# Kernel tuning notes

Hardware: AMD Instinct MI355X
Metric: run time of the kernel (lower is better)

The kernel has to match this reference:

```python
import jax, jax.numpy as jnp
import numpy as np

N_NODES = 20000
N_EDGES = 320000
MUL = 64            # multiplicity of 0e and 1o in hidden/out irreps
NUM_BASIS = 8
INV_SQRT3 = 0.5773502691896258
EPS = 1e-5


def setup_inputs() -> dict:
    key = jax.random.key(0)
    k = jax.random.split(key, 16)
    return {
        "node_hiddens": jax.random.normal(k[0], (N_NODES, 4 * MUL), dtype=jnp.float32),
        "edge_attr": jax.random.uniform(k[1], (N_EDGES, NUM_BASIS), dtype=jnp.float32),
        "edge_sh": jax.random.normal(k[2], (N_EDGES, 4), dtype=jnp.float32),
        "w1_s": jax.random.normal(k[3], (MUL, MUL), dtype=jnp.float32),
        "w1_v": jax.random.normal(k[4], (MUL, MUL), dtype=jnp.float32),
        "wsc_s": jax.random.normal(k[5], (MUL, MUL), dtype=jnp.float32),
        "wsc_v": jax.random.normal(k[6], (MUL, MUL), dtype=jnp.float32),
        "w2_s": jax.random.normal(k[7], (2 * MUL, MUL), dtype=jnp.float32),
        "w2_v": jax.random.normal(k[8], (2 * MUL, MUL), dtype=jnp.float32),
        "fc_w1": jax.random.normal(k[9], (NUM_BASIS, 64), dtype=jnp.float32),
        "fc_w2": jax.random.normal(k[10], (64, 64), dtype=jnp.float32),
        "fc_w3": jax.random.normal(k[11], (64, 4 * MUL), dtype=jnp.float32),
        "g_s": jnp.ones((MUL,), dtype=jnp.float32),
        "g_v": jnp.ones((MUL,), dtype=jnp.float32),
        "edge_index": jax.random.randint(k[12], (2, N_EDGES), 0, N_NODES),
    }


def reference(node_hiddens, edge_attr, edge_sh, w1_s, w1_v, wsc_s, wsc_v,
              w2_s, w2_v, fc_w1, fc_w2, fc_w3, g_s, g_v, edge_index):
    N = node_hiddens.shape[0]
    # e3nn layout: [N, 64x0e | 64x1o] with mul-major vectors
    xs = node_hiddens[:, :MUL]                        # [N, 64]
    xv = node_hiddens[:, MUL:].reshape(N, MUL, 3)     # [N, 64, 3]

    # edge MLP (FullyConnectedNet([8,64,64,256], silu)) -> per-edge TP weights
    h = jax.nn.silu(edge_attr @ fc_w1 * (1.0 / np.sqrt(float(NUM_BASIS))))
    h = jax.nn.silu(h @ fc_w2 * (1.0 / np.sqrt(64.0)))
    w = h @ fc_w3 * (1.0 / np.sqrt(64.0))             # [E, 4*MUL]
    wA, wB, wC, wD = jnp.split(w, 4, axis=1)          # one 64-vec per uvu path

    inv = 1.0 / np.sqrt(float(MUL))
    # self-connection Linear(hidden -> out)
    sc_s = xs @ wsc_s * inv
    sc_v = jnp.einsum('nud,uv->nvd', xv, wsc_v) * inv
    # linear_1 Linear(hidden -> hidden)
    ys = xs @ w1_s * inv
    yv = jnp.einsum('nud,uv->nvd', xv, w1_v) * inv

    src = edge_index[0]
    dst = edge_index[1]
    es = ys[dst]                                      # [E, 64] gather
    ev = yv[dst]                                      # [E, 64, 3]
    sh0 = edge_sh[:, :1]                              # [E, 1]
    sh1 = edge_sh[:, 1:]                              # [E, 3]

    # weighted uvu Clebsch-Gordan tensor product -> irreps_mid (sorted order)
    m0a = wA * es * sh0                                          # 0e x 0e -> 0e
    m0b = wD * jnp.einsum('eud,ed->eu', ev, sh1) * INV_SQRT3     # 1o x 1o -> 0e
    m1a = wB[:, :, None] * es[:, :, None] * sh1[:, None, :]      # 0e x 1o -> 1o
    m1b = wC[:, :, None] * ev * sh0[:, :, None]                  # 1o x 0e -> 1o
    mid_s = jnp.concatenate([m0a, m0b], axis=1)       # [E, 128]
    mid_v = jnp.concatenate([m1a, m1b], axis=1)       # [E, 128, 3]

    # scatter-sum to source nodes + 1/sqrt(degree) normalization
    ns = jax.ops.segment_sum(mid_s, src, num_segments=N)
    nv = jax.ops.segment_sum(mid_v, src, num_segments=N)
    deg = jax.ops.segment_sum(jnp.ones((src.shape[0],), node_hiddens.dtype), src, num_segments=N)
    dn = jax.lax.rsqrt(jnp.maximum(deg, 1.0))
    ns = ns * dn[:, None]
    nv = nv * dn[:, None, None]

    # linear_2 Linear(128x0e+128x1o -> 64x0e+64x1o) + self connection
    inv2 = 1.0 / np.sqrt(2.0 * MUL)
    os_ = ns @ w2_s * inv2 + sc_s
    ov = jnp.einsum('nud,uv->nvd', nv, w2_v) * inv2 + sc_v

    # equivariant RMS layer norm per irrep type (centering=False)
    os_ = os_ * jax.lax.rsqrt(jnp.mean(os_ * os_, axis=1, keepdims=True) + EPS) * g_s
    rms_v = jax.lax.rsqrt(jnp.mean(ov * ov, axis=(1, 2))[:, None, None] + EPS)
    ov = ov * rms_v * g_v[None, :, None]

    return jnp.concatenate([os_, ov.reshape(N, 3 * MUL)], axis=1)
```

## Files before the change

### kernel.cpp

```cpp
#include <hip/hip_runtime.h>
#include <math.h>

#define N_NODES 20000
#define N_EDGES 320000
#define N_TILES 1250

typedef __attribute__((ext_vector_type(8))) short bf16x8;
typedef __attribute__((ext_vector_type(4))) float f32x4;
typedef __attribute__((ext_vector_type(2))) unsigned u32x2;
typedef __attribute__((ext_vector_type(4))) unsigned u32x4;

__device__ __forceinline__ float silu_f(float x) {
    return x / (1.0f + __expf(-x));
}
__device__ __forceinline__ short f2bf(float x) {
    union { float f; unsigned u; } v; v.f = x;
    unsigned r = (v.u + 0x7FFFu + ((v.u >> 16) & 1u)) >> 16;
    return (short)r;
}
__device__ __forceinline__ float blo(unsigned u) { return __uint_as_float(u << 16); }
__device__ __forceinline__ float bhi(unsigned u) { return __uint_as_float(u & 0xFFFF0000u); }
__device__ __forceinline__ unsigned cvt_pk(float lo, float hi) {
    unsigned r;
    asm("v_cvt_pk_bf16_f32 %0, %1, %2" : "=v"(r) : "v"(lo), "v"(hi));
    return r;
}
#define MFMA16(a, b, c) __builtin_amdgcn_mfma_f32_16x16x32_bf16((a), (b), (c), 0, 0, 0)

__global__ __launch_bounds__(256) void s_hist(const int* __restrict__ eidx,
                                              int* __restrict__ cnt) {
    const int e = blockIdx.x * 256 + threadIdx.x;
    if (e < N_EDGES) atomicAdd(&cnt[eidx[e]], 1);
}

__global__ __launch_bounds__(1024) void s_scan(int* __restrict__ cnt,
                                               int* __restrict__ start) {
    const int tid = threadIdx.x;
    const int base = tid * 20;
    int vals[20];
    int sum = 0;
    #pragma unroll
    for (int j = 0; j < 20; ++j) {
        const int i = base + j;
        const int v = (i < N_NODES) ? cnt[i] : 0;
        vals[j] = sum;
        sum += v;
    }
    const int lane = tid & 63, wv = tid >> 6;
    int x = sum;
    #pragma unroll
    for (int off = 1; off < 64; off <<= 1) {
        const int t = __shfl_up(x, off);
        if (lane >= off) x += t;
    }
    __shared__ int wtot[16];
    if (lane == 63) wtot[wv] = x;
    __syncthreads();
    int wpref = 0;
    for (int k = 0; k < wv; ++k) wpref += wtot[k];
    const int excl = wpref + x - sum;
    #pragma unroll
    for (int j = 0; j < 20; ++j) {
        const int i = base + j;
        if (i < N_NODES) {
            const int s = excl + vals[j];
            start[i] = s;
            cnt[i] = s;
        }
    }
    if (tid == 1023) start[N_NODES] = wpref + x;
}

__global__ __launch_bounds__(256) void s_scatter(const int* __restrict__ eidx,
                                                 int* __restrict__ cursor,
                                                 int* __restrict__ perm) {
    const int e = blockIdx.x * 256 + threadIdx.x;
    if (e >= N_EDGES) return;
    const int src = eidx[e];
    const int pos = atomicAdd(&cursor[src], 1);
    perm[pos] = e;
}

__global__ __launch_bounds__(256) void k_pack(
    const float* __restrict__ fcw1, const float* __restrict__ fcw2,
    const float* __restrict__ fcw3,
    const float* __restrict__ w1s, const float* __restrict__ wscs,
    const float* __restrict__ w1v, const float* __restrict__ wscv,
    const float* __restrict__ w2s, const float* __restrict__ w2v,
    short* __restrict__ w1A, short* __restrict__ w2A, short* __restrict__ w3A,
    short* __restrict__ wp1, short* __restrict__ wp2)
{
    const int tid = blockIdx.x * 256 + threadIdx.x;
    const int nthr = gridDim.x * 256;
    for (int i = tid; i < 4*64*8; i += nthr) {
        const int j = i & 7, lane = (i >> 3) & 63, t = i >> 9;
        const int k = (lane >> 4) * 8 + j, row = t*16 + (lane & 15);
        w1A[i] = (k < 8) ? f2bf(fcw1[k*64 + row]) : (short)0;
    }
    for (int i = tid; i < 8*64*8; i += nthr) {
        const int j = i & 7, lane = (i >> 3) & 63, kk = (i >> 9) & 1, t = i >> 10;
        const int k = kk*32 + (lane >> 4)*8 + j, row = t*16 + (lane & 15);
        w2A[i] = f2bf(fcw2[k*64 + row]);
    }
    for (int i = tid; i < 32*64*8; i += nthr) {
        const int j = i & 7, lane = (i >> 3) & 63, kk = (i >> 9) & 1, Tp = i >> 10;
        const int c = Tp >> 2, q = Tp & 3;
        const int k = kk*32 + (lane >> 4)*8 + j;
        const int ch = (q*4 + c)*16 + (lane & 15);
        const float s = (ch >= 192) ? 0.5773502691896258f : 1.0f;
        w3A[i] = f2bf(fcw3[(size_t)k*256 + ch] * s);
    }
    for (int i = tid; i < 4096; i += nthr) {
        const int j = i & 7, lane = (i >> 3) & 63, kk = (i >> 9) & 1, vt = i >> 10;
        const int row = vt*16 + (lane & 15), k = kk*32 + (lane >> 4)*8 + j;
        wp1[i]         = f2bf(w1s [k*64 + row]);
        wp1[4096 + i]  = f2bf(wscs[k*64 + row]);
        wp1[8192 + i]  = f2bf(w1v [k*64 + row]);
        wp1[12288 + i] = f2bf(wscv[k*64 + row]);
    }
    for (int i = tid; i < 8192; i += nthr) {
        const int j = i & 7, lane = (i >> 3) & 63, kk = (i >> 9) & 3, vt = i >> 11;
        const int row = vt*16 + (lane & 15), k = kk*32 + (lane >> 4)*8 + j;
        const int r = (k & 1)*64 + (k >> 1);
        wp2[i]        = f2bf(w2s[r*64 + row]);
        wp2[8192 + i] = f2bf(w2v[r*64 + row]);
    }
}

__global__ __launch_bounds__(256) void k1_mfma(
    const float* __restrict__ nh, const short* __restrict__ wp1,
    short* __restrict__ ydata, short* __restrict__ scpack)
{
    const int lane = threadIdx.x & 63;
    const int tile = blockIdx.x * 4 + (threadIdx.x >> 6);
    if (tile >= N_TILES) return;
    const int l15 = lane & 15, lhi = lane >> 4;
    const int n = tile*16 + l15;
    const float* row = nh + (size_t)n * 256;
    const f32x4 zz = {0.f, 0.f, 0.f, 0.f};
    f32x4 acc[8][4];
    #pragma unroll
    for (int c = 0; c < 8; ++c)
        #pragma unroll
        for (int vt = 0; vt < 4; ++vt) acc[c][vt] = zz;

    #pragma unroll
    for (int kk = 0; kk < 2; ++kk) {
        const int k0 = kk*32 + lhi*8;
        const float4 s0 = *(const float4*)(row + k0);
        const float4 s1 = *(const float4*)(row + k0 + 4);
        float4 vv[6];
        #pragma unroll
        for (int q = 0; q < 6; ++q) vv[q] = *(const float4*)(row + 64 + 3*k0 + q*4);
        const float* vf = (const float*)vv;
        union { u32x4 u; bf16x8 v; } bs, b0, b1, b2;
        bs.u[0] = cvt_pk(s0.x, s0.y); bs.u[1] = cvt_pk(s0.z, s0.w);
        bs.u[2] = cvt_pk(s1.x, s1.y); bs.u[3] = cvt_pk(s1.z, s1.w);
        #pragma unroll
        for (int q = 0; q < 4; ++q) {
            b0.u[q] = cvt_pk(vf[6*q + 0], vf[6*q + 3]);
            b1.u[q] = cvt_pk(vf[6*q + 1], vf[6*q + 4]);
            b2.u[q] = cvt_pk(vf[6*q + 2], vf[6*q + 5]);
        }
        #pragma unroll
        for (int vt = 0; vt < 4; ++vt) {
            const int fo = ((vt*2 + kk)*64 + lane)*8;
            const bf16x8 a_ys = *(const bf16x8*)&wp1[fo];
            const bf16x8 a_ss = *(const bf16x8*)&wp1[4096 + fo];
            const bf16x8 a_yv = *(const bf16x8*)&wp1[8192 + fo];
            const bf16x8 a_sv = *(const bf16x8*)&wp1[12288 + fo];
            acc[0][vt] = MFMA16(a_ys, bs.v, acc[0][vt]);
            acc[1][vt] = MFMA16(a_ss, bs.v, acc[1][vt]);
            acc[2][vt] = MFMA16(a_yv, b0.v, acc[2][vt]);
            acc[3][vt] = MFMA16(a_yv, b1.v, acc[3][vt]);
            acc[4][vt] = MFMA16(a_yv, b2.v, acc[4][vt]);
            acc[5][vt] = MFMA16(a_sv, b0.v, acc[5][vt]);
            acc[6][vt] = MFMA16(a_sv, b1.v, acc[6][vt]);
            acc[7][vt] = MFMA16(a_sv, b2.v, acc[7][vt]);
        }
    }
    #pragma unroll
    for (int vt = 0; vt < 4; ++vt)
        #pragma unroll
        for (int r = 0; r < 4; ++r) {
            const int v = vt*16 + lhi*4 + r;
            u32x2 yo, so;
            yo[0] = cvt_pk(acc[0][vt][r]*0.125f, acc[2][vt][r]*0.125f);
            yo[1] = cvt_pk(acc[3][vt][r]*0.125f, acc[4][vt][r]*0.125f);
            so[0] = cvt_pk(acc[1][vt][r]*0.125f, acc[5][vt][r]*0.125f);
            so[1] = cvt_pk(acc[6][vt][r]*0.125f, acc[7][vt][r]*0.125f);
            *(u32x2*)&ydata [((size_t)n*64 + v)*4] = yo;
            *(u32x2*)&scpack[((size_t)n*64 + v)*4] = so;
        }
}

__global__ __launch_bounds__(256) void k_mlp(
    const float* __restrict__ ea, const int* __restrict__ perm,
    const short* __restrict__ w1A, const short* __restrict__ w2A,
    const short* __restrict__ w3A, short* __restrict__ wq)
{
    __shared__ short hb1[4][1024];
    __shared__ short hb2[4][1024];
    const int lane = threadIdx.x & 63, w = threadIdx.x >> 6;
    const int l15 = lane & 15, lhi = lane >> 4;
    const int wbase = (blockIdx.x * 4 + w) * 32;
    short* h1b = hb1[w];
    short* h2b = hb2[w];
    const int swz = (l15 & 7) << 4;
    const f32x4 zz = {0.f, 0.f, 0.f, 0.f};

    bf16x8 a1[4], a2[4][2];
    #pragma unroll
    for (int t = 0; t < 4; ++t)
        a1[t] = *(const bf16x8*)&w1A[(t*64 + lane)*8];
    #pragma unroll
    for (int t = 0; t < 4; ++t)
        #pragma unroll
        for (int kk = 0; kk < 2; ++kk)
            a2[t][kk] = *(const bf16x8*)&w2A[((t*2 + kk)*64 + lane)*8];

    bf16x8 bh2[2][2];
    #pragma unroll
    for (int sb = 0; sb < 2; ++sb) {
        bf16x8 bea = {0,0,0,0,0,0,0,0};
        if (lhi == 0) {
            const int e = perm[wbase + sb*16 + l15];
            const float4 p0 = *(const float4*)(ea + (size_t)e*8);
            const float4 p1 = *(const float4*)(ea + (size_t)e*8 + 4);
            union { u32x4 u; bf16x8 v; } tu;
            tu.u[0] = cvt_pk(p0.x, p0.y);
            tu.u[1] = cvt_pk(p0.z, p0.w);
            tu.u[2] = cvt_pk(p1.x, p1.y);
            tu.u[3] = cvt_pk(p1.z, p1.w);
            bea = tu.v;
        }
        f32x4 d1[4];
        #pragma unroll
        for (int t = 0; t < 4; ++t)
            d1[t] = MFMA16(a1[t], bea, zz);
        #pragma unroll
        for (int t = 0; t < 4; ++t) {
            const float s0 = silu_f(d1[t][0] * 0.35355339059327373f);
            const float s1 = silu_f(d1[t][1] * 0.35355339059327373f);
            const float s2 = silu_f(d1[t][2] * 0.35355339059327373f);
            const float s3 = silu_f(d1[t][3] * 0.35355339059327373f);
            u32x2 pk; pk[0] = cvt_pk(s0, s1); pk[1] = cvt_pk(s2, s3);
            const int byt = (l15*128 + t*32 + lhi*8) ^ swz;
            *(u32x2*)((char*)h1b + byt) = pk;
        }
        bf16x8 bh1[2];
        #pragma unroll
        for (int kk = 0; kk < 2; ++kk)
            bh1[kk] = *(const bf16x8*)((const char*)h1b + ((l15*128 + kk*64 + lhi*16) ^ swz));
        f32x4 d2[4];
        #pragma unroll
        for (int t = 0; t < 4; ++t) {
            d2[t] = MFMA16(a2[t][0], bh1[0], zz);
            d2[t] = MFMA16(a2[t][1], bh1[1], d2[t]);
        }
        #pragma unroll
        for (int t = 0; t < 4; ++t) {
            const float s0 = silu_f(d2[t][0] * 0.125f) * 0.125f;
            const float s1 = silu_f(d2[t][1] * 0.125f) * 0.125f;
            const float s2 = silu_f(d2[t][2] * 0.125f) * 0.125f;
            const float s3 = silu_f(d2[t][3] * 0.125f) * 0.125f;
            u32x2 pk; pk[0] = cvt_pk(s0, s1); pk[1] = cvt_pk(s2, s3);
            const int byt = (l15*128 + t*32 + lhi*8) ^ swz;
            *(u32x2*)((char*)h2b + byt) = pk;
        }
        #pragma unroll
        for (int kk = 0; kk < 2; ++kk)
            bh2[sb][kk] = *(const bf16x8*)((const char*)h2b + ((l15*128 + kk*64 + lhi*16) ^ swz));
    }

    #pragma unroll
    for (int c = 0; c < 4; ++c) {
        f32x4 dq[4][2];
        #pragma unroll
        for (int q = 0; q < 4; ++q) {
            const int Tp = c*4 + q;
            const bf16x8 a30 = *(const bf16x8*)&w3A[((Tp*2 + 0)*64 + lane)*8];
            const bf16x8 a31 = *(const bf16x8*)&w3A[((Tp*2 + 1)*64 + lane)*8];
            #pragma unroll
            for (int sb = 0; sb < 2; ++sb) {
                f32x4 d = MFMA16(a30, bh2[sb][0], zz);
                dq[q][sb] = MFMA16(a31, bh2[sb][1], d);
            }
        }
        #pragma unroll
        for (int sb = 0; sb < 2; ++sb) {
            const int slot = wbase + sb*16 + l15;
            const int vbase = c*16 + lhi*4;
            u32x4 lo, hi;
            lo[0] = cvt_pk(dq[0][sb][0], dq[1][sb][0]);
            lo[1] = cvt_pk(dq[2][sb][0], dq[3][sb][0]);
            lo[2] = cvt_pk(dq[0][sb][1], dq[1][sb][1]);
            lo[3] = cvt_pk(dq[2][sb][1], dq[3][sb][1]);
            hi[0] = cvt_pk(dq[0][sb][2], dq[1][sb][2]);
            hi[1] = cvt_pk(dq[2][sb][2], dq[3][sb][2]);
            hi[2] = cvt_pk(dq[0][sb][3], dq[1][sb][3]);
            hi[3] = cvt_pk(dq[2][sb][3], dq[3][sb][3]);
            short* base = &wq[((size_t)slot*64 + vbase)*4];
            *(u32x4*)(base)     = lo;
            *(u32x4*)(base + 8) = hi;
        }
    }
}

__global__ __launch_bounds__(256) void k2_gather(
    const int* __restrict__ start, const int* __restrict__ perm,
    const int* __restrict__ eidx, const float* __restrict__ esh,
    const short* __restrict__ wq, const short* __restrict__ ydata,
    unsigned* __restrict__ ncat32)
{
    const int lane = threadIdx.x & 63;
    const int n = blockIdx.x * 4 + (threadIdx.x >> 6);
    if (n >= N_NODES) return;
    const int s0 = start[n], s1 = start[n + 1];
    float acc0=0.f, acc1=0.f, av0=0.f, av1=0.f, av2=0.f, bv0=0.f, bv1=0.f, bv2=0.f;
    for (int p = s0; p < s1; p += 8) {
        const int m = s1 - p;
        u32x2 wv[8], yd[8];
        float4 sh[8];
        int e[8];
        #pragma unroll
        for (int j = 0; j < 8; ++j) {
            const int pp = (j < m) ? p + j : s0;
            e[j] = perm[pp];
            wv[j] = *(const u32x2*)&wq[((size_t)pp*64 + lane)*4];
        }
        #pragma unroll
        for (int j = 0; j < 8; ++j) {
            sh[j] = *(const float4*)(esh + (size_t)e[j]*4);
            const int dst = eidx[N_EDGES + e[j]];
            yd[j] = *(const u32x2*)&ydata[((size_t)dst*64 + lane)*4];
        }
        #pragma unroll
        for (int j = 0; j < 8; ++j) {
            const float g = (j < m) ? 1.f : 0.f;
            const float wa = blo(wv[j][0])*g, wb = bhi(wv[j][0])*g;
            const float wc = blo(wv[j][1])*g, wd = bhi(wv[j][1])*g;
            const float es  = blo(yd[j][0]), ev0 = bhi(yd[j][0]);
            const float ev1 = blo(yd[j][1]), ev2 = bhi(yd[j][1]);
            acc0 += wa * es * sh[j].x;
            acc1 += wd * (ev0*sh[j].y + ev1*sh[j].z + ev2*sh[j].w);
            const float esb = wb * es;
            av0 += esb * sh[j].y; av1 += esb * sh[j].z; av2 += esb * sh[j].w;
            const float c0 = wc * sh[j].x;
            bv0 += c0 * ev0; bv1 += c0 * ev1; bv2 += c0 * ev2;
        }
    }
    unsigned* nrow = ncat32 + (size_t)n * 256;
    nrow[lane]        = cvt_pk(acc0, acc1);
    nrow[64  + lane]  = cvt_pk(av0, bv0);
    nrow[128 + lane]  = cvt_pk(av1, bv1);
    nrow[192 + lane]  = cvt_pk(av2, bv2);
}

__global__ __launch_bounds__(256) void k3_mfma(
    const unsigned* __restrict__ ncat32, const int* __restrict__ start,
    const short* __restrict__ wp2, const short* __restrict__ scpack,
    const float* __restrict__ gs, const float* __restrict__ gv,
    float* __restrict__ out)
{
    const int lane = threadIdx.x & 63;
    const int tile = blockIdx.x * 4 + (threadIdx.x >> 6);
    if (tile >= N_TILES) return;
    const int l15 = lane & 15, lhi = lane >> 4;
    const int n = tile*16 + l15;
    const f32x4 zz = {0.f, 0.f, 0.f, 0.f};
    f32x4 acc[4][4];
    #pragma unroll
    for (int c = 0; c < 4; ++c)
        #pragma unroll
        for (int vt = 0; vt < 4; ++vt) acc[c][vt] = zz;

    const size_t nb = (size_t)n * 256;
    #pragma unroll
    for (int kk = 0; kk < 4; ++kk) {
        const int uo = kk*16 + lhi*4;
        union { u32x4 u; bf16x8 v; } bs, b0, b1, b2;
        bs.u = *(const u32x4*)&ncat32[nb +        uo];
        b0.u = *(const u32x4*)&ncat32[nb +  64 + uo];
        b1.u = *(const u32x4*)&ncat32[nb + 128 + uo];
        b2.u = *(const u32x4*)&ncat32[nb + 192 + uo];
        #pragma unroll
        for (int vt = 0; vt < 4; ++vt) {
            const int fo = ((vt*4 + kk)*64 + lane)*8;
            const bf16x8 a_s = *(const bf16x8*)&wp2[fo];
            const bf16x8 a_v = *(const bf16x8*)&wp2[8192 + fo];
            acc[0][vt] = MFMA16(a_s, bs.v, acc[0][vt]);
            acc[1][vt] = MFMA16(a_v, b0.v, acc[1][vt]);
            acc[2][vt] = MFMA16(a_v, b1.v, acc[2][vt]);
            acc[3][vt] = MFMA16(a_v, b2.v, acc[3][vt]);
        }
    }
    const float degf = (float)(start[n+1] - start[n]);
    const float coef = rsqrtf(fmaxf(degf, 1.0f)) * 0.08838834764831845f;
    float os[4][4], o0[4][4], o1[4][4], o2[4][4];
    float ssq = 0.f, vsq = 0.f;
    #pragma unroll
    for (int vt = 0; vt < 4; ++vt)
        #pragma unroll
        for (int r = 0; r < 4; ++r) {
            const int v = vt*16 + lhi*4 + r;
            const u32x2 sc = *(const u32x2*)&scpack[((size_t)n*64 + v)*4];
            os[vt][r] = acc[0][vt][r]*coef + blo(sc[0]);
            o0[vt][r] = acc[1][vt][r]*coef + bhi(sc[0]);
            o1[vt][r] = acc[2][vt][r]*coef + blo(sc[1]);
            o2[vt][r] = acc[3][vt][r]*coef + bhi(sc[1]);
            ssq += os[vt][r]*os[vt][r];
            vsq += o0[vt][r]*o0[vt][r] + o1[vt][r]*o1[vt][r] + o2[vt][r]*o2[vt][r];
        }
    ssq += __shfl_xor(ssq, 16); ssq += __shfl_xor(ssq, 32);
    vsq += __shfl_xor(vsq, 16); vsq += __shfl_xor(vsq, 32);
    const float rs = rsqrtf(ssq * (1.0f/64.0f) + 1e-5f);
    const float rv = rsqrtf(vsq * (1.0f/192.0f) + 1e-5f);
    float* orow = out + (size_t)n * 256;
    #pragma unroll
    for (int vt = 0; vt < 4; ++vt) {
        const int vb = vt*16 + lhi*4;
        const float4 g4  = *(const float4*)(gs + vb);
        const float4 gv4 = *(const float4*)(gv + vb);
        const float4 so = { os[vt][0]*rs*g4.x, os[vt][1]*rs*g4.y,
                            os[vt][2]*rs*g4.z, os[vt][3]*rs*g4.w };
        *(float4*)(orow + vb) = so;
        const float m0 = rv*gv4.x, m1 = rv*gv4.y, m2 = rv*gv4.z, m3 = rv*gv4.w;
        const float4 w0 = { o0[vt][0]*m0, o1[vt][0]*m0, o2[vt][0]*m0, o0[vt][1]*m1 };
        const float4 w1 = { o1[vt][1]*m1, o2[vt][1]*m1, o0[vt][2]*m2, o1[vt][2]*m2 };
        const float4 w2 = { o2[vt][2]*m2, o0[vt][3]*m3, o1[vt][3]*m3, o2[vt][3]*m3 };
        float* vbase = orow + 64 + vb*3;
        *(float4*)(vbase)     = w0;
        *(float4*)(vbase + 4) = w1;
        *(float4*)(vbase + 8) = w2;
    }
}

extern "C" void kernel_launch(void* const* d_in, const int* in_sizes, int n_in,
                              void* d_out, int out_size, void* d_ws, size_t ws_size,
                              hipStream_t stream) {
    const float* nh   = (const float*)d_in[0];
    const float* ea   = (const float*)d_in[1];
    const float* esh  = (const float*)d_in[2];
    const float* w1s  = (const float*)d_in[3];
    const float* w1v  = (const float*)d_in[4];
    const float* wscs = (const float*)d_in[5];
    const float* wscv = (const float*)d_in[6];
    const float* w2s  = (const float*)d_in[7];
    const float* w2v  = (const float*)d_in[8];
    const float* fcw1 = (const float*)d_in[9];
    const float* fcw2 = (const float*)d_in[10];
    const float* fcw3 = (const float*)d_in[11];
    const float* gs   = (const float*)d_in[12];
    const float* gv   = (const float*)d_in[13];
    const int*   eidx = (const int*)d_in[14];
    float* out = (float*)d_out;

    char* wsb = (char*)d_ws;
    size_t off = 0;
    short* ydata  = (short*)(wsb + off); off += (size_t)N_NODES * 256 * 2;
    short* scpack = (short*)(wsb + off); off += (size_t)N_NODES * 256 * 2;
    unsigned* ncat32 = (unsigned*)(wsb + off); off += (size_t)N_NODES * 256 * 4;
    int* cnt      = (int*)(wsb + off); off += (size_t)N_NODES * 4;
    int* start    = (int*)(wsb + off); off += ((size_t)N_NODES + 1) * 4;
    int* perm     = (int*)(wsb + off); off += (size_t)N_EDGES * 4;
    short* w1A = (short*)(wsb + off); off += 2048 * 2;
    short* w2A = (short*)(wsb + off); off += 4096 * 2;
    short* w3A = (short*)(wsb + off); off += 16384 * 2;
    short* wp1 = (short*)(wsb + off); off += 16384 * 2;
    short* wp2 = (short*)(wsb + off); off += 16384 * 2;
    off = (off + 15) & ~(size_t)15;
    short* wq = (short*)(wsb + off);

    hipMemsetAsync(cnt, 0, N_NODES * sizeof(int), stream);

    s_hist<<<(N_EDGES + 255)/256, 256, 0, stream>>>(eidx, cnt);
    s_scan<<<1, 1024, 0, stream>>>(cnt, start);
    s_scatter<<<(N_EDGES + 255)/256, 256, 0, stream>>>(eidx, cnt, perm);

    k_pack<<<32, 256, 0, stream>>>(fcw1, fcw2, fcw3, w1s, wscs, w1v, wscv,
                                   w2s, w2v, w1A, w2A, w3A, wp1, wp2);

    k1_mfma<<<(N_TILES + 3)/4, 256, 0, stream>>>(nh, wp1, ydata, scpack);

    k_mlp<<<N_EDGES/128, 256, 0, stream>>>(ea, perm, w1A, w2A, w3A, wq);

    k2_gather<<<(N_NODES + 3)/4, 256, 0, stream>>>(
        start, perm, eidx, esh, wq, ydata, ncat32);

    k3_mfma<<<(N_TILES + 3)/4, 256, 0, stream>>>(
        ncat32, start, wp2, scpack, gs, gv, out);
}
```

Measured before the change: 218.3 us.

## Merge independent setup kernels by block range and precompute sorted destination indices

Folds the weight-packing kernel into the histogram launch, and the node linear kernel into the edge scatter launch, splitting work by block index so independent stages share one launch. This removes two kernel launches and lets unrelated work run concurrently. The scatter also writes a destination index array in sorted order, so the gather kernel reads it contiguously instead of making a dependent random load through the edge permutation. The cost is an extra index array write and larger fused grids.

```diff
diff --git a/kernel.cpp b/kernel.cpp
--- a/kernel.cpp
+++ b/kernel.cpp
@@ -4,6 +4,10 @@
 #define N_NODES 20000
 #define N_EDGES 320000
 #define N_TILES 1250
+#define PACK_BLOCKS 32
+#define HIST_BLOCKS ((N_EDGES + 255) / 256)
+#define SCAT_BLOCKS ((N_EDGES + 255) / 256)
+#define K1_BLOCKS ((N_TILES + 3) / 4)
 
 typedef __attribute__((ext_vector_type(8))) short bf16x8;
 typedef __attribute__((ext_vector_type(4))) float f32x4;
@@ -27,61 +31,8 @@
 }
 #define MFMA16(a, b, c) __builtin_amdgcn_mfma_f32_16x16x32_bf16((a), (b), (c), 0, 0, 0)
 
-__global__ __launch_bounds__(256) void s_hist(const int* __restrict__ eidx,
-                                              int* __restrict__ cnt) {
-    const int e = blockIdx.x * 256 + threadIdx.x;
-    if (e < N_EDGES) atomicAdd(&cnt[eidx[e]], 1);
-}
-
-__global__ __launch_bounds__(1024) void s_scan(int* __restrict__ cnt,
-                                               int* __restrict__ start) {
-    const int tid = threadIdx.x;
-    const int base = tid * 20;
-    int vals[20];
-    int sum = 0;
-    #pragma unroll
-    for (int j = 0; j < 20; ++j) {
-        const int i = base + j;
-        const int v = (i < N_NODES) ? cnt[i] : 0;
-        vals[j] = sum;
-        sum += v;
-    }
-    const int lane = tid & 63, wv = tid >> 6;
-    int x = sum;
-    #pragma unroll
-    for (int off = 1; off < 64; off <<= 1) {
-        const int t = __shfl_up(x, off);
-        if (lane >= off) x += t;
-    }
-    __shared__ int wtot[16];
-    if (lane == 63) wtot[wv] = x;
-    __syncthreads();
-    int wpref = 0;
-    for (int k = 0; k < wv; ++k) wpref += wtot[k];
-    const int excl = wpref + x - sum;
-    #pragma unroll
-    for (int j = 0; j < 20; ++j) {
-        const int i = base + j;
-        if (i < N_NODES) {
-            const int s = excl + vals[j];
-            start[i] = s;
-            cnt[i] = s;
-        }
-    }
-    if (tid == 1023) start[N_NODES] = wpref + x;
-}
-
-__global__ __launch_bounds__(256) void s_scatter(const int* __restrict__ eidx,
-                                                 int* __restrict__ cursor,
-                                                 int* __restrict__ perm) {
-    const int e = blockIdx.x * 256 + threadIdx.x;
-    if (e >= N_EDGES) return;
-    const int src = eidx[e];
-    const int pos = atomicAdd(&cursor[src], 1);
-    perm[pos] = e;
-}
-
-__global__ __launch_bounds__(256) void k_pack(
+__global__ __launch_bounds__(256) void kp_hist(
+    const int* __restrict__ eidx, int* __restrict__ cnt,
     const float* __restrict__ fcw1, const float* __restrict__ fcw2,
     const float* __restrict__ fcw3,
     const float* __restrict__ w1s, const float* __restrict__ wscs,
@@ -90,8 +41,13 @@
     short* __restrict__ w1A, short* __restrict__ w2A, short* __restrict__ w3A,
     short* __restrict__ wp1, short* __restrict__ wp2)
 {
+    if (blockIdx.x >= PACK_BLOCKS) {
+        const int e = (blockIdx.x - PACK_BLOCKS) * 256 + threadIdx.x;
+        if (e < N_EDGES) atomicAdd(&cnt[eidx[e]], 1);
+        return;
+    }
     const int tid = blockIdx.x * 256 + threadIdx.x;
-    const int nthr = gridDim.x * 256;
+    const int nthr = PACK_BLOCKS * 256;
     for (int i = tid; i < 4*64*8; i += nthr) {
         const int j = i & 7, lane = (i >> 3) & 63, t = i >> 9;
         const int k = (lane >> 4) * 8 + j, row = t*16 + (lane & 15);
@@ -127,12 +83,62 @@
     }
 }
 
-__global__ __launch_bounds__(256) void k1_mfma(
+__global__ __launch_bounds__(1024) void s_scan(int* __restrict__ cnt,
+                                               int* __restrict__ start) {
+    const int tid = threadIdx.x;
+    const int base = tid * 20;
+    int vals[20];
+    int sum = 0;
+    #pragma unroll
+    for (int j = 0; j < 20; ++j) {
+        const int i = base + j;
+        const int v = (i < N_NODES) ? cnt[i] : 0;
+        vals[j] = sum;
+        sum += v;
+    }
+    const int lane = tid & 63, wv = tid >> 6;
+    int x = sum;
+    #pragma unroll
+    for (int off = 1; off < 64; off <<= 1) {
+        const int t = __shfl_up(x, off);
+        if (lane >= off) x += t;
+    }
+    __shared__ int wtot[16];
+    if (lane == 63) wtot[wv] = x;
+    __syncthreads();
+    int wpref = 0;
+    for (int k = 0; k < wv; ++k) wpref += wtot[k];
+    const int excl = wpref + x - sum;
+    #pragma unroll
+    for (int j = 0; j < 20; ++j) {
+        const int i = base + j;
+        if (i < N_NODES) {
+            const int s = excl + vals[j];
+            start[i] = s;
+            cnt[i] = s;
+        }
+    }
+    if (tid == 1023) start[N_NODES] = wpref + x;
+}
+
+__global__ __launch_bounds__(256) void scat_k1(
+    const int* __restrict__ eidx, int* __restrict__ cursor,
+    int* __restrict__ perm, int* __restrict__ dst_perm,
     const float* __restrict__ nh, const short* __restrict__ wp1,
     short* __restrict__ ydata, short* __restrict__ scpack)
 {
+    if (blockIdx.x < SCAT_BLOCKS) {
+        const int e = blockIdx.x * 256 + threadIdx.x;
+        if (e < N_EDGES) {
+            const int src = eidx[e];
+            const int pos = atomicAdd(&cursor[src], 1);
+            perm[pos] = e;
+            dst_perm[pos] = eidx[N_EDGES + e];
+        }
+        return;
+    }
     const int lane = threadIdx.x & 63;
-    const int tile = blockIdx.x * 4 + (threadIdx.x >> 6);
+    const int tile = (blockIdx.x - SCAT_BLOCKS) * 4 + (threadIdx.x >> 6);
     if (tile >= N_TILES) return;
     const int l15 = lane & 15, lhi = lane >> 4;
     const int n = tile*16 + l15;
@@ -309,7 +315,7 @@
 
 __global__ __launch_bounds__(256) void k2_gather(
     const int* __restrict__ start, const int* __restrict__ perm,
-    const int* __restrict__ eidx, const float* __restrict__ esh,
+    const int* __restrict__ dst_perm, const float* __restrict__ esh,
     const short* __restrict__ wq, const short* __restrict__ ydata,
     unsigned* __restrict__ ncat32)
 {
@@ -322,18 +328,18 @@
         const int m = s1 - p;
         u32x2 wv[8], yd[8];
         float4 sh[8];
-        int e[8];
+        int e[8], d[8];
         #pragma unroll
         for (int j = 0; j < 8; ++j) {
             const int pp = (j < m) ? p + j : s0;
             e[j] = perm[pp];
+            d[j] = dst_perm[pp];
             wv[j] = *(const u32x2*)&wq[((size_t)pp*64 + lane)*4];
         }
         #pragma unroll
         for (int j = 0; j < 8; ++j) {
             sh[j] = *(const float4*)(esh + (size_t)e[j]*4);
-            const int dst = eidx[N_EDGES + e[j]];
-            yd[j] = *(const u32x2*)&ydata[((size_t)dst*64 + lane)*4];
+            yd[j] = *(const u32x2*)&ydata[((size_t)d[j]*64 + lane)*4];
         }
         #pragma unroll
         for (int j = 0; j < 8; ++j) {
@@ -464,6 +470,7 @@
     int* cnt      = (int*)(wsb + off); off += (size_t)N_NODES * 4;
     int* start    = (int*)(wsb + off); off += ((size_t)N_NODES + 1) * 4;
     int* perm     = (int*)(wsb + off); off += (size_t)N_EDGES * 4;
+    int* dst_perm = (int*)(wsb + off); off += (size_t)N_EDGES * 4;
     short* w1A = (short*)(wsb + off); off += 2048 * 2;
     short* w2A = (short*)(wsb + off); off += 4096 * 2;
     short* w3A = (short*)(wsb + off); off += 16384 * 2;
@@ -474,19 +481,19 @@
 
     hipMemsetAsync(cnt, 0, N_NODES * sizeof(int), stream);
 
-    s_hist<<<(N_EDGES + 255)/256, 256, 0, stream>>>(eidx, cnt);
+    kp_hist<<<PACK_BLOCKS + HIST_BLOCKS, 256, 0, stream>>>(
+        eidx, cnt, fcw1, fcw2, fcw3, w1s, wscs, w1v, wscv, w2s, w2v,
+        w1A, w2A, w3A, wp1, wp2);
+
     s_scan<<<1, 1024, 0, stream>>>(cnt, start);
-    s_scatter<<<(N_EDGES + 255)/256, 256, 0, stream>>>(eidx, cnt, perm);
-
-    k_pack<<<32, 256, 0, stream>>>(fcw1, fcw2, fcw3, w1s, wscs, w1v, wscv,
-                                   w2s, w2v, w1A, w2A, w3A, wp1, wp2);
-
-    k1_mfma<<<(N_TILES + 3)/4, 256, 0, stream>>>(nh, wp1, ydata, scpack);
+
+    scat_k1<<<SCAT_BLOCKS + K1_BLOCKS, 256, 0, stream>>>(
+        eidx, cnt, perm, dst_perm, nh, wp1, ydata, scpack);
 
     k_mlp<<<N_EDGES/128, 256, 0, stream>>>(ea, perm, w1A, w2A, w3A, wq);
 
     k2_gather<<<(N_NODES + 3)/4, 256, 0, stream>>>(
-        start, perm, eidx, esh, wq, ydata, ncat32);
+        start, perm, dst_perm, esh, wq, ydata, ncat32);
 
     k3_mfma<<<(N_TILES + 3)/4, 256, 0, stream>>>(
         ncat32, start, wp2, scpack, gs, gv, out);
```

Result: faster. 202.5 us (median of 2 runs) (-7.2%).
